# Performance work log

Measured on AMD Instinct MI355X. Metric: run time of the kernel, lower is better.

The kernel has to match this reference:

```python
import jax, jax.numpy as jnp
import numpy as np

N_NODES = 100000
N_EDGES = 3200000
N_FEAT = 128
HIDDEN = 64
N_GRAPHS = 512
N_CLASSES = 10


def setup_inputs() -> dict:
    key = jax.random.key(0)
    ks = jax.random.split(key, 12)
    x = jax.random.normal(ks[0], (N_NODES, N_FEAT), dtype=jnp.float32)
    edge_index = jax.random.randint(ks[1], (2, N_EDGES), 0, N_NODES, dtype=jnp.int64 if jax.config.jax_enable_x64 else jnp.int32)
    batch = jnp.sort(jax.random.randint(ks[2], (N_NODES,), 0, N_GRAPHS, dtype=jnp.int32))
    def glorot(k, shape):
        lim = float(np.sqrt(6.0 / (shape[0] + shape[1])))
        return jax.random.uniform(k, shape, jnp.float32, -lim, lim)
    return {
        'x': x, 'edge_index': edge_index, 'batch': batch,
        'W1': glorot(ks[3], (N_FEAT, HIDDEN)), 'b1': jnp.zeros((HIDDEN,), jnp.float32),
        'W2': glorot(ks[4], (HIDDEN, HIDDEN)), 'b2': jnp.zeros((HIDDEN,), jnp.float32),
        'W3': glorot(ks[5], (HIDDEN, HIDDEN)), 'b3': jnp.zeros((HIDDEN,), jnp.float32),
        'Wc1': glorot(ks[6], (HIDDEN, 32)), 'bc1': jnp.zeros((32,), jnp.float32),
        'Wc2': glorot(ks[7], (32, N_CLASSES)), 'bc2': jnp.zeros((N_CLASSES,), jnp.float32),
    }


def _gcn_conv(x, W, b, src, dst, norm):
    # x' = scatter_add_{dst}( norm * (x @ W)[src] ) + b   (self-loops included in src/dst)
    h = x @ W  # [N, H]
    msg = h[src] * norm[:, None]  # gather + edge scale: [E+N, H]
    out = jax.ops.segment_sum(msg, dst, num_segments=N_NODES)
    return out + b


def reference(x, edge_index, batch, W1, b1, W2, b2, W3, b3, Wc1, bc1, Wc2, bc2):
    n = x.shape[0]
    loop = jnp.arange(n, dtype=edge_index.dtype)
    src = jnp.concatenate([edge_index[0], loop])
    dst = jnp.concatenate([edge_index[1], loop])
    # symmetric gcn_norm: deg over target nodes (incl. self-loops)
    deg = jax.ops.segment_sum(jnp.ones_like(dst, dtype=x.dtype), dst, num_segments=n)
    dinv = jnp.where(deg > 0, jax.lax.rsqrt(jnp.maximum(deg, 1.0)), 0.0)
    norm = dinv[src] * dinv[dst]  # [E+N]

    h = jax.nn.relu(_gcn_conv(x, W1, b1, src, dst, norm))
    h = jax.nn.relu(_gcn_conv(h, W2, b2, src, dst, norm))
    h = jax.nn.relu(_gcn_conv(h, W3, b3, src, dst, norm))

    # global_mean_pool over batch ids
    sums = jax.ops.segment_sum(h, batch, num_segments=N_GRAPHS)
    cnts = jax.ops.segment_sum(jnp.ones((n,), h.dtype), batch, num_segments=N_GRAPHS)
    pooled = sums / jnp.maximum(cnts, 1.0)[:, None]  # [G, H]

    # classifier (dropout inactive at eval)
    z = jax.nn.relu(pooled @ Wc1 + bc1)
    return z @ Wc2 + bc2
```

## Files before the change

### kernel.cpp

```cpp
#include <hip/hip_runtime.h>
#include <hip/hip_bf16.h>


typedef unsigned short u16;
typedef float f32x2 __attribute__((ext_vector_type(2)));

__device__ __forceinline__ u16 f2bf(float f) {
    unsigned int x = __float_as_uint(f);
    return (u16)((x + 0x7fffu + ((x >> 16) & 1u)) >> 16);
}

__device__ __forceinline__ void pk_acc(f32x2& p, unsigned int v) {
    f32x2 u;
    u[0] = __uint_as_float(v << 16);
    u[1] = __uint_as_float(v & 0xffff0000u);
    asm("v_pk_add_f32 %0, %0, %1" : "+v"(p) : "v"(u));
}
__device__ __forceinline__ void addrow_pk(const uint4 v, f32x2& p0, f32x2& p1,
                                          f32x2& p2, f32x2& p3) {
    pk_acc(p0, v.x); pk_acc(p1, v.y); pk_acc(p2, v.z); pk_acc(p3, v.w);
}

#define BMAX 2048
#define NBLK 256

__global__ __launch_bounds__(1024) void part_hist(const int* __restrict__ dst,
                                                  int* __restrict__ cntmat,
                                                  int E, int B, int chunk) {
    __shared__ int hist[BMAX];
    for (int i = threadIdx.x; i < BMAX; i += 1024) hist[i] = 0;
    __syncthreads();
    int s = blockIdx.x * chunk;
    int en = min(s + chunk, E);
    for (int i = s + threadIdx.x; i < en; i += 1024)
        atomicAdd(&hist[dst[i] >> 6], 1);
    __syncthreads();
    for (int i = threadIdx.x; i < B; i += 1024)
        cntmat[i * NBLK + blockIdx.x] = hist[i];
}

__global__ __launch_bounds__(256) void part_scan(int* __restrict__ cntmat,
                                                 int* __restrict__ bcnt, int B) {
    int w = threadIdx.x >> 6;
    int lane = threadIdx.x & 63;
    int b = blockIdx.x * 4 + w;
    if (b >= B) return;
    int carry = 0;
#pragma unroll
    for (int j = 0; j < NBLK / 64; j++) {
        int idx = b * NBLK + j * 64 + lane;
        int v = cntmat[idx];
        int x = v;
#pragma unroll
        for (int d = 1; d < 64; d <<= 1) {
            int t = __shfl_up(x, d, 64);
            if (lane >= d) x += t;
        }
        cntmat[idx] = x - v + carry;
        carry += __shfl(x, 63, 64);
    }
    if (lane == 0) bcnt[b] = carry;
}

__global__ __launch_bounds__(256) void bucket_scan(const int* __restrict__ bcnt,
                                                   int* __restrict__ prp, int M) {
    __shared__ int lds[256];
    int t = threadIdx.x;
    int base = t * 8;
    int v[8]; int ts = 0;
#pragma unroll
    for (int i = 0; i < 8; i++) { int idx = base + i; int x = (idx < M) ? bcnt[idx] : 0; v[i] = x; ts += x; }
    lds[t] = ts; __syncthreads();
#pragma unroll
    for (int d = 1; d < 256; d <<= 1) {
        int x = (t >= d) ? lds[t - d] : 0; __syncthreads();
        lds[t] += x; __syncthreads();
    }
    int run = lds[t] - ts;
#pragma unroll
    for (int i = 0; i < 8; i++) {
        int idx = base + i;
        if (idx < M) { prp[idx] = run; run += v[i]; }
    }
    if (t == 255) prp[M] = lds[255];
}

__global__ __launch_bounds__(1024) void part_scatter(const int* __restrict__ src,
                                                     const int* __restrict__ dst,
                                                     const int* __restrict__ cntmat,
                                                     const int* __restrict__ prp,
                                                     int* __restrict__ pairs,
                                                     int E, int B, int chunk) {
    __shared__ int cur[BMAX];
    for (int i = threadIdx.x; i < B; i += 1024)
        cur[i] = prp[i] + cntmat[i * NBLK + blockIdx.x];
    __syncthreads();
    int s = blockIdx.x * chunk;
    int en = min(s + chunk, E);
    for (int i = s + threadIdx.x; i < en; i += 1024) {
        int d = dst[i];
        int pos = atomicAdd(&cur[d >> 6], 1);
        pairs[pos] = src[i] | ((d & 63) << 17);
    }
}

__global__ __launch_bounds__(256) void csr_build(const int* __restrict__ pairs,
                                                 const int* __restrict__ prp,
                                                 int* __restrict__ rp,
                                                 float* __restrict__ dinv,
                                                 int* __restrict__ csr,
                                                 int N, int B, int E) {
    __shared__ int hist[64], cur[64];
    int b = blockIdx.x;
    int t = threadIdx.x;
    if (t < 64) hist[t] = 0;
    __syncthreads();
    int r0 = prp[b], r1 = prp[b + 1];
    for (int i = r0 + t; i < r1; i += 256)
        atomicAdd(&hist[pairs[i] >> 17], 1);
    __syncthreads();
    if (t == 0) {
        int run = r0;
        for (int k = 0; k < 64; k++) { cur[k] = run; run += hist[k]; }
    }
    __syncthreads();
    if (t < 64) {
        int node = b * 64 + t;
        if (node < N) {
            rp[node] = cur[t];
            dinv[node] = rsqrtf((float)(hist[t] + 1));
        }
    }
    if (b == B - 1 && t == 0) rp[N] = E;
    __syncthreads();
    for (int i = r0 + t; i < r1; i += 256) {
        int v = pairs[i];
        int pos = atomicAdd(&cur[v >> 17], 1);
        csr[pos] = v & 0x1FFFF;
    }
}

template <int K>
__global__ __launch_bounds__(256) void gemm_dinv(const float* __restrict__ X,
                                                 const float* __restrict__ W,
                                                 const float* __restrict__ dinv,
                                                 unsigned int* __restrict__ G2, int N) {
    constexpr int ROWS = 64;
    __shared__ float Xl[ROWS * K];
    int tid = threadIdx.x;
    int c   = tid & 31;
    int rh  = (tid >> 5) & 1;
    int wid = tid >> 6;
    int row0 = blockIdx.x * ROWS;
    const float* xsrc = X + (size_t)row0 * K;

    if (row0 + ROWS <= N) {
#pragma unroll
        for (int i = tid; i < ROWS * K / 4; i += 256)
            ((float4*)Xl)[i] = ((const float4*)xsrc)[i];
    } else {
        int avail = (N - row0) * K;
        for (int i = tid; i < ROWS * K; i += 256)
            Xl[i] = (i < avail) ? xsrc[i] : 0.f;
    }
    __syncthreads();

    float2 acc[8];
#pragma unroll
    for (int p = 0; p < 8; p++) { acc[p].x = 0.f; acc[p].y = 0.f; }
    const float2* W2 = (const float2*)W;

#pragma unroll 1
    for (int ck = 0; ck < K / 16; ck++) {
        float2 w[16];
#pragma unroll
        for (int k = 0; k < 16; k++) w[k] = W2[(ck * 16 + k) * 32 + c];
#pragma unroll
        for (int p = 0; p < 8; p++) {
            const float* xrow = &Xl[(wid * 16 + p * 2 + rh) * K + ck * 16];
#pragma unroll
            for (int k4 = 0; k4 < 4; k4++) {
                float4 xv = *(const float4*)&xrow[k4 * 4];
                acc[p].x = fmaf(xv.x, w[k4 * 4 + 0].x, acc[p].x);
                acc[p].y = fmaf(xv.x, w[k4 * 4 + 0].y, acc[p].y);
                acc[p].x = fmaf(xv.y, w[k4 * 4 + 1].x, acc[p].x);
                acc[p].y = fmaf(xv.y, w[k4 * 4 + 1].y, acc[p].y);
                acc[p].x = fmaf(xv.z, w[k4 * 4 + 2].x, acc[p].x);
                acc[p].y = fmaf(xv.z, w[k4 * 4 + 2].y, acc[p].y);
                acc[p].x = fmaf(xv.w, w[k4 * 4 + 3].x, acc[p].x);
                acc[p].y = fmaf(xv.w, w[k4 * 4 + 3].y, acc[p].y);
            }
        }
    }
#pragma unroll
    for (int p = 0; p < 8; p++) {
        int row = row0 + wid * 16 + p * 2 + rh;
        if (row < N) {
            float dn = dinv[row];
            unsigned int lo = f2bf(dn * acc[p].x);
            unsigned int hi = f2bf(dn * acc[p].y);
            G2[(size_t)row * 32 + c] = lo | (hi << 16);
        }
    }
}

__global__ __launch_bounds__(256) void aggregate(const unsigned int* __restrict__ G,
                                                 const int* __restrict__ rp,
                                                 const int* __restrict__ csr,
                                                 const float* __restrict__ dinv,
                                                 const float* __restrict__ bias,
                                                 float* __restrict__ H, int N) {
    int node = blockIdx.x * 4 + (threadIdx.x >> 6);
    if (node >= N) return;
    node = __builtin_amdgcn_readfirstlane(node);
    int lane = threadIdx.x & 63;
    int grp = lane >> 3, sub = lane & 7;
    int beg = rp[node], end = rp[node + 1];
    const char* Gb = (const char*)G;
    unsigned int so = (unsigned int)sub << 4;

    f32x2 p0 = {0.f, 0.f}, p1 = {0.f, 0.f}, p2 = {0.f, 0.f}, p3 = {0.f, 0.f};
    if (grp == 0) {
        uint4 v = *(const uint4*)(Gb + (((unsigned int)node << 7) + so));
        addrow_pk(v, p0, p1, p2, p3);
    }

    int e = beg + grp;
    for (; e + 24 < end; e += 32) {
        unsigned int o0 = ((unsigned int)csr[e] << 7) + so;
        unsigned int o1 = ((unsigned int)csr[e + 8] << 7) + so;
        unsigned int o2 = ((unsigned int)csr[e + 16] << 7) + so;
        unsigned int o3 = ((unsigned int)csr[e + 24] << 7) + so;
        uint4 v0 = *(const uint4*)(Gb + o0);
        uint4 v1 = *(const uint4*)(Gb + o1);
        uint4 v2 = *(const uint4*)(Gb + o2);
        uint4 v3 = *(const uint4*)(Gb + o3);
        addrow_pk(v0, p0, p1, p2, p3); addrow_pk(v1, p0, p1, p2, p3);
        addrow_pk(v2, p0, p1, p2, p3); addrow_pk(v3, p0, p1, p2, p3);
    }
    if (e + 8 < end) {
        unsigned int o0 = ((unsigned int)csr[e] << 7) + so;
        unsigned int o1 = ((unsigned int)csr[e + 8] << 7) + so;
        uint4 v0 = *(const uint4*)(Gb + o0);
        uint4 v1 = *(const uint4*)(Gb + o1);
        addrow_pk(v0, p0, p1, p2, p3); addrow_pk(v1, p0, p1, p2, p3);
        e += 16;
    }
    for (; e < end; e += 8) {
        uint4 v = *(const uint4*)(Gb + (((unsigned int)csr[e] << 7) + so));
        addrow_pk(v, p0, p1, p2, p3);
    }

#pragma unroll
    for (int m = 8; m <= 32; m <<= 1) {
        p0[0] += __shfl_xor(p0[0], m, 64); p0[1] += __shfl_xor(p0[1], m, 64);
        p1[0] += __shfl_xor(p1[0], m, 64); p1[1] += __shfl_xor(p1[1], m, 64);
        p2[0] += __shfl_xor(p2[0], m, 64); p2[1] += __shfl_xor(p2[1], m, 64);
        p3[0] += __shfl_xor(p3[0], m, 64); p3[1] += __shfl_xor(p3[1], m, 64);
    }
    if (grp == 0) {
        float dn = dinv[node];
        float4 ba = ((const float4*)bias)[sub * 2];
        float4 bb = ((const float4*)bias)[sub * 2 + 1];
        float4 r0, r1;
        r0.x = fmaxf(fmaf(dn, p0[0], ba.x), 0.f);
        r0.y = fmaxf(fmaf(dn, p0[1], ba.y), 0.f);
        r0.z = fmaxf(fmaf(dn, p1[0], ba.z), 0.f);
        r0.w = fmaxf(fmaf(dn, p1[1], ba.w), 0.f);
        r1.x = fmaxf(fmaf(dn, p2[0], bb.x), 0.f);
        r1.y = fmaxf(fmaf(dn, p2[1], bb.y), 0.f);
        r1.z = fmaxf(fmaf(dn, p3[0], bb.z), 0.f);
        r1.w = fmaxf(fmaf(dn, p3[1], bb.w), 0.f);
        ((float4*)H)[(size_t)node * 16 + sub * 2]     = r0;
        ((float4*)H)[(size_t)node * 16 + sub * 2 + 1] = r1;
    }
}

__global__ __launch_bounds__(256) void pool_classify(const float* __restrict__ H,
                                                     const int* __restrict__ batch,
                                                     const float* __restrict__ Wc1,
                                                     const float* __restrict__ bc1,
                                                     const float* __restrict__ Wc2,
                                                     const float* __restrict__ bc2,
                                                     float* __restrict__ out,
                                                     int N) {
    int g = blockIdx.x;
    int t = threadIdx.x & 63;
    int w = threadIdx.x >> 6;
    __shared__ float psum[4][64];
    __shared__ float p[64];
    __shared__ float z[32];

    int lo = 0, hi = N;
    while (lo < hi) { int m = (lo + hi) >> 1; if (batch[m] < g) lo = m + 1; else hi = m; }
    int start = lo;
    int lo2 = start, hi2 = N;
    while (lo2 < hi2) { int m = (lo2 + hi2) >> 1; if (batch[m] < g + 1) lo2 = m + 1; else hi2 = m; }
    int end = lo2;

    float acc = 0.f;
    for (int n = start + w; n < end; n += 4) acc += H[(size_t)n * 64 + t];
    psum[w][t] = acc;
    __syncthreads();
    if (w == 0) {
        float inv = 1.0f / fmaxf((float)(end - start), 1.0f);
        p[t] = (psum[0][t] + psum[1][t] + psum[2][t] + psum[3][t]) * inv;
    }
    __syncthreads();
    if (threadIdx.x < 32) {
        float a = bc1[threadIdx.x];
        for (int f = 0; f < 64; f++) a = fmaf(p[f], Wc1[f * 32 + threadIdx.x], a);
        z[threadIdx.x] = fmaxf(a, 0.f);
    }
    __syncthreads();
    if (threadIdx.x < 10) {
        float a = bc2[threadIdx.x];
        for (int j = 0; j < 32; j++) a = fmaf(z[j], Wc2[j * 10 + threadIdx.x], a);
        out[(size_t)g * 10 + threadIdx.x] = a;
    }
}

extern "C" void kernel_launch(void* const* d_in, const int* in_sizes, int n_in,
                              void* d_out, int out_size, void* d_ws, size_t ws_size,
                              hipStream_t stream) {
    const float* x   = (const float*)d_in[0];
    const int*   ei  = (const int*)d_in[1];
    const int*   bat = (const int*)d_in[2];
    const float* W1  = (const float*)d_in[3];
    const float* b1  = (const float*)d_in[4];
    const float* W2  = (const float*)d_in[5];
    const float* b2  = (const float*)d_in[6];
    const float* W3  = (const float*)d_in[7];
    const float* b3  = (const float*)d_in[8];
    const float* Wc1 = (const float*)d_in[9];
    const float* bc1 = (const float*)d_in[10];
    const float* Wc2 = (const float*)d_in[11];
    const float* bc2 = (const float*)d_in[12];

    const int N  = in_sizes[0] / 128;
    const int E  = in_sizes[1] / 2;
    const int NG = out_size / 10;
    const int B  = (N + 63) >> 6;
    const int* srcp = ei;
    const int* dstp = ei + E;

    char* ws = (char*)d_ws;
    size_t off = 0;
    auto alloc = [&](size_t bytes) -> void* {
        void* p = ws + off;
        off += (bytes + 255) / 256 * 256;
        return p;
    };
    unsigned int* G = (unsigned int*)alloc((size_t)N * 32 * 4);
    float* H      = (float*)alloc((size_t)N * 64 * 4);
    int*   pairs  = (int*)H;
    int*   csr    = (int*)alloc((size_t)E * 4);
    int*   rp     = (int*)alloc((size_t)(N + 1) * 4);
    float* dinv   = (float*)alloc((size_t)N * 4);
    int*   bcnt   = (int*)alloc((size_t)BMAX * 4);
    int*   prp    = (int*)alloc((size_t)(BMAX + 1) * 4);
    int*   cntmat = (int*)alloc((size_t)BMAX * NBLK * 4);
    (void)ws_size; (void)n_in;

    const int chunk = (E + NBLK - 1) / NBLK;
    part_hist<<<NBLK, 1024, 0, stream>>>(dstp, cntmat, E, B, chunk);
    part_scan<<<(B + 3) / 4, 256, 0, stream>>>(cntmat, bcnt, B);
    bucket_scan<<<1, 256, 0, stream>>>(bcnt, prp, B);
    part_scatter<<<NBLK, 1024, 0, stream>>>(srcp, dstp, cntmat, prp, pairs, E, B, chunk);
    csr_build<<<B, 256, 0, stream>>>(pairs, prp, rp, dinv, csr, N, B, E);

    gemm_dinv<128><<<(N + 63) / 64, 256, 0, stream>>>(x, W1, dinv, G, N);
    aggregate<<<(N + 3) / 4, 256, 0, stream>>>(G, rp, csr, dinv, b1, H, N);
    gemm_dinv<64><<<(N + 63) / 64, 256, 0, stream>>>(H, W2, dinv, G, N);
    aggregate<<<(N + 3) / 4, 256, 0, stream>>>(G, rp, csr, dinv, b2, H, N);
    gemm_dinv<64><<<(N + 63) / 64, 256, 0, stream>>>(H, W3, dinv, G, N);
    aggregate<<<(N + 3) / 4, 256, 0, stream>>>(G, rp, csr, dinv, b3, H, N);

    pool_classify<<<NG, 256, 0, stream>>>(H, bat, Wc1, bc1, Wc2, bc2, (float*)d_out, N);
}
```

Before: 456.4 us.

## Process two nodes per wavefront in GCN aggregation with deeper edge unroll

The aggregate kernel now maps two destination nodes per 64-lane wavefront: each half-wave of 32 lanes uses 4 edge groups of 8 lanes instead of 8 groups for one node. The main loop keeps 8 gathers in flight per lane, and the reduction drops one shuffle stage. With an average degree of about 33, this aims to cut idle lanes in the tail iterations and halve the launched blocks. The node index is no longer wave-uniform, so the readfirstlane scalarization is lost. The packed-add inline asm is also replaced with plain scalar float adds.

After: 472.0 us. +3.4%, slower.

```diff
diff --git a/kernel.cpp b/kernel.cpp
--- a/kernel.cpp
+++ b/kernel.cpp
@@ -11,10 +11,8 @@
 }
 
 __device__ __forceinline__ void pk_acc(f32x2& p, unsigned int v) {
-    f32x2 u;
-    u[0] = __uint_as_float(v << 16);
-    u[1] = __uint_as_float(v & 0xffff0000u);
-    asm("v_pk_add_f32 %0, %0, %1" : "+v"(p) : "v"(u));
+    p[0] += __uint_as_float(v << 16);
+    p[1] += __uint_as_float(v & 0xffff0000u);
 }
 __device__ __forceinline__ void addrow_pk(const uint4 v, f32x2& p0, f32x2& p1,
                                           f32x2& p2, f32x2& p3) {
@@ -210,11 +208,12 @@
                                                  const float* __restrict__ dinv,
                                                  const float* __restrict__ bias,
                                                  float* __restrict__ H, int N) {
-    int node = blockIdx.x * 4 + (threadIdx.x >> 6);
+    int lane = threadIdx.x & 63;
+    int h    = lane >> 5;
+    int node = blockIdx.x * 8 + (threadIdx.x >> 6) * 2 + h;
     if (node >= N) return;
-    node = __builtin_amdgcn_readfirstlane(node);
-    int lane = threadIdx.x & 63;
-    int grp = lane >> 3, sub = lane & 7;
+    int grp = (lane >> 3) & 3;
+    int sub = lane & 7;
     int beg = rp[node], end = rp[node + 1];
     const char* Gb = (const char*)G;
     unsigned int so = (unsigned int)sub << 4;
@@ -226,33 +225,42 @@
     }
 
     int e = beg + grp;
-    for (; e + 24 < end; e += 32) {
-        unsigned int o0 = ((unsigned int)csr[e] << 7) + so;
-        unsigned int o1 = ((unsigned int)csr[e + 8] << 7) + so;
-        unsigned int o2 = ((unsigned int)csr[e + 16] << 7) + so;
-        unsigned int o3 = ((unsigned int)csr[e + 24] << 7) + so;
-        uint4 v0 = *(const uint4*)(Gb + o0);
-        uint4 v1 = *(const uint4*)(Gb + o1);
-        uint4 v2 = *(const uint4*)(Gb + o2);
-        uint4 v3 = *(const uint4*)(Gb + o3);
+    for (; e + 28 < end; e += 32) {
+        uint4 v0 = *(const uint4*)(Gb + (((unsigned int)csr[e]      << 7) + so));
+        uint4 v1 = *(const uint4*)(Gb + (((unsigned int)csr[e + 4]  << 7) + so));
+        uint4 v2 = *(const uint4*)(Gb + (((unsigned int)csr[e + 8]  << 7) + so));
+        uint4 v3 = *(const uint4*)(Gb + (((unsigned int)csr[e + 12] << 7) + so));
+        uint4 v4 = *(const uint4*)(Gb + (((unsigned int)csr[e + 16] << 7) + so));
+        uint4 v5 = *(const uint4*)(Gb + (((unsigned int)csr[e + 20] << 7) + so));
+        uint4 v6 = *(const uint4*)(Gb + (((unsigned int)csr[e + 24] << 7) + so));
+        uint4 v7 = *(const uint4*)(Gb + (((unsigned int)csr[e + 28] << 7) + so));
         addrow_pk(v0, p0, p1, p2, p3); addrow_pk(v1, p0, p1, p2, p3);
         addrow_pk(v2, p0, p1, p2, p3); addrow_pk(v3, p0, p1, p2, p3);
-    }
-    if (e + 8 < end) {
-        unsigned int o0 = ((unsigned int)csr[e] << 7) + so;
-        unsigned int o1 = ((unsigned int)csr[e + 8] << 7) + so;
-        uint4 v0 = *(const uint4*)(Gb + o0);
-        uint4 v1 = *(const uint4*)(Gb + o1);
+        addrow_pk(v4, p0, p1, p2, p3); addrow_pk(v5, p0, p1, p2, p3);
+        addrow_pk(v6, p0, p1, p2, p3); addrow_pk(v7, p0, p1, p2, p3);
+    }
+    if (e + 12 < end) {
+        uint4 v0 = *(const uint4*)(Gb + (((unsigned int)csr[e]      << 7) + so));
+        uint4 v1 = *(const uint4*)(Gb + (((unsigned int)csr[e + 4]  << 7) + so));
+        uint4 v2 = *(const uint4*)(Gb + (((unsigned int)csr[e + 8]  << 7) + so));
+        uint4 v3 = *(const uint4*)(Gb + (((unsigned int)csr[e + 12] << 7) + so));
         addrow_pk(v0, p0, p1, p2, p3); addrow_pk(v1, p0, p1, p2, p3);
+        addrow_pk(v2, p0, p1, p2, p3); addrow_pk(v3, p0, p1, p2, p3);
         e += 16;
     }
-    for (; e < end; e += 8) {
+    if (e + 4 < end) {
+        uint4 v0 = *(const uint4*)(Gb + (((unsigned int)csr[e]     << 7) + so));
+        uint4 v1 = *(const uint4*)(Gb + (((unsigned int)csr[e + 4] << 7) + so));
+        addrow_pk(v0, p0, p1, p2, p3); addrow_pk(v1, p0, p1, p2, p3);
+        e += 8;
+    }
+    for (; e < end; e += 4) {
         uint4 v = *(const uint4*)(Gb + (((unsigned int)csr[e] << 7) + so));
         addrow_pk(v, p0, p1, p2, p3);
     }
 
 #pragma unroll
-    for (int m = 8; m <= 32; m <<= 1) {
+    for (int m = 8; m <= 16; m <<= 1) {
         p0[0] += __shfl_xor(p0[0], m, 64); p0[1] += __shfl_xor(p0[1], m, 64);
         p1[0] += __shfl_xor(p1[0], m, 64); p1[1] += __shfl_xor(p1[1], m, 64);
         p2[0] += __shfl_xor(p2[0], m, 64); p2[1] += __shfl_xor(p2[1], m, 64);
@@ -370,11 +378,11 @@
     csr_build<<<B, 256, 0, stream>>>(pairs, prp, rp, dinv, csr, N, B, E);
 
     gemm_dinv<128><<<(N + 63) / 64, 256, 0, stream>>>(x, W1, dinv, G, N);
-    aggregate<<<(N + 3) / 4, 256, 0, stream>>>(G, rp, csr, dinv, b1, H, N);
+    aggregate<<<(N + 7) / 8, 256, 0, stream>>>(G, rp, csr, dinv, b1, H, N);
     gemm_dinv<64><<<(N + 63) / 64, 256, 0, stream>>>(H, W2, dinv, G, N);
-    aggregate<<<(N + 3) / 4, 256, 0, stream>>>(G, rp, csr, dinv, b2, H, N);
+    aggregate<<<(N + 7) / 8, 256, 0, stream>>>(G, rp, csr, dinv, b2, H, N);
     gemm_dinv<64><<<(N + 63) / 64, 256, 0, stream>>>(H, W3, dinv, G, N);
-    aggregate<<<(N + 3) / 4, 256, 0, stream>>>(G, rp, csr, dinv, b3, H, N);
+    aggregate<<<(N + 7) / 8, 256, 0, stream>>>(G, rp, csr, dinv, b3, H, N);
 
     pool_classify<<<NG, 256, 0, stream>>>(H, bat, Wc1, bc1, Wc2, bc2, (float*)d_out, N);
 }
```
